# Kernel tuning notes

Hardware: AMD Instinct MI355X
Metric: run time of the kernel (lower is better)

The kernel has to match this reference:

```python
import jax, jax.numpy as jnp
import numpy as np
from math import comb

N_DEGREE = 3  # init kwarg n


def _exponent_nk(n, K):
    # Faithful port of exponent_nk: exponent rows of all degree-n monomials in K vars.
    ident = np.diag(np.ones(K))
    exp = ident
    for i in range(1, n):
        rows = []
        for j in range(K):
            for k in range(exp.shape[0] - comb(i + K - j - 1, i), exp.shape[0]):
                rows.append(ident[j, :] + exp[k, :])
        exp = np.stack(rows, axis=0)
    return exp


def _mono_indices(powers):
    # For each exponent row, list the variable indices with multiplicity (deg entries).
    M, K = powers.shape
    deg = int(powers[0].sum())
    idx = np.zeros((M, deg), dtype=np.int32)
    for i in range(M):
        c = 0
        for j in range(K):
            for _ in range(int(powers[i, j])):
                idx[i, c] = j
                c += 1
    return idx


def _generate_veronese(x, n):
    # x: (K, N). Returns (D, N) with rows [1; x; deg2 monomials; ...; degn monomials].
    K, N = x.shape
    parts = [jnp.ones((1, N), x.dtype), x]
    for deg in range(2, n + 1):
        idx = _mono_indices(_exponent_nk(deg, K))  # (M, deg) static int indices
        y = x[idx[:, 0]]  # (M, N)
        for t in range(1, deg):
            y = y * x[idx[:, t]]
        parts.append(y)
    return jnp.concatenate(parts, axis=0)


def reference(x, M_inv):
    npoints, dims = x.shape
    # Faithful to torch: .view is a row-major reshape, NOT a transpose.
    xr = jnp.reshape(x, (dims, npoints))
    v = _generate_veronese(xr, N_DEGREE)  # (D, N)
    D, N = v.shape
    vq = jnp.reshape(v, (N, D))  # faithful replica of v_x.view(BS, 1, D)
    t = vq @ M_inv               # (N, D)
    out = jnp.sum(t * vq, axis=1)  # (N,) quadratic form v^T M_inv v
    return out.reshape(N, 1, 1)


def setup_inputs() -> dict:
    key = jax.random.key(0)
    k1, k2 = jax.random.split(key)
    npoints, dims = 262144, 10
    D = comb(dims + N_DEGREE, N_DEGREE)  # 286
    x = jax.random.normal(k1, (npoints, dims), dtype=jnp.float32)
    M_inv = jax.random.normal(k2, (D, D), dtype=jnp.float32)
    return {"x": x, "M_inv": M_inv}
```

## Files before the change

kernel.cpp:

```cpp
#include <hip/hip_runtime.h>
#include <hip/hip_bf16.h>
#include <stdint.h>

#define NLOG 18
#define NMASK ((1u << NLOG) - 1u)
#define RSTRB 592u
#define ROWS 32u
#define TPB 384u
#define MPB (ROWS * 286u)

typedef __attribute__((ext_vector_type(8))) short short8;
typedef __attribute__((ext_vector_type(4))) float f32x4;
typedef f32x4 uf32x4 __attribute__((aligned(4)));

struct Tab { uint16_t v[286]; };
constexpr Tab make_tab() {
  Tab t{};
  int idx = 0;
  t.v[idx++] = 0;
  for (int a = 0; a < 10; ++a) t.v[idx++] = (uint16_t)(a + 1);
  for (int a = 0; a < 10; ++a)
    for (int b = a; b < 10; ++b) t.v[idx++] = (uint16_t)((a + 1) | ((b + 1) << 4));
  for (int a = 0; a < 10; ++a)
    for (int b = a; b < 10; ++b)
      for (int c = b; c < 10; ++c)
        t.v[idx++] = (uint16_t)((a + 1) | ((b + 1) << 4) | ((c + 1) << 8));
  return t;
}
__constant__ Tab g_tab = make_tab();

__device__ uint4 g_bpack[11520];

__device__ __forceinline__ uint32_t f2bf(float f) {
  uint32_t u = __float_as_uint(f);
  return (u + 0x7FFFu + ((u >> 16) & 1u)) >> 16;
}
__device__ __forceinline__ float bf2f(uint32_t u) { return __uint_as_float(u << 16); }
__device__ __forceinline__ uint32_t pk2bf(float lo, float hi) {
  __hip_bfloat162 h2 = __float22bfloat162_rn(make_float2(lo, hi));
  return *(uint32_t*)&h2;
}

__global__ __launch_bounds__(256) void prep_kernel(const float* __restrict__ M) {
  uint32_t t = blockIdx.x * 256u + threadIdx.x;
  uint32_t k0 = t / 1280u;
  uint32_t r = t - k0 * 1280u;
  uint32_t g = r / 320u;
  uint32_t e = r - g * 320u;
  uint32_t kb = k0 * 32u + g * 8u;
  float v[8];
#pragma unroll
  for (int i = 0; i < 8; ++i) {
    uint32_t k = kb + (uint32_t)i;
    v[i] = (k < 286u && e < 286u) ? M[k * 286u + e] : 0.f;
  }
  uint4 o;
  o.x = f2bf(v[0]) | (f2bf(v[1]) << 16);
  o.y = f2bf(v[2]) | (f2bf(v[3]) << 16);
  o.z = f2bf(v[4]) | (f2bf(v[5]) << 16);
  o.w = f2bf(v[6]) | (f2bf(v[7]) << 16);
  g_bpack[t] = o;
}

__device__ __forceinline__ float mono1(const float* __restrict__ x, uint32_t tv, uint32_t j) {
  float val = 1.f;
  int a = (int)(tv & 15u) - 1;
  if (a >= 0) {
    val = x[((uint32_t)a << NLOG) + j];
    int b = (int)((tv >> 4) & 15u) - 1;
    if (b >= 0) {
      val *= x[((uint32_t)b << NLOG) + j];
      int c = (int)(tv >> 8) - 1;
      if (c >= 0) val *= x[((uint32_t)c << NLOG) + j];
    }
  }
  return val;
}

__global__ __launch_bounds__(TPB, 6) void qform_kernel(const float* __restrict__ x,
                                                       float* __restrict__ out) {
  extern __shared__ char smem[];
  float* part = (float*)(smem + 18944);

  const uint32_t tid = threadIdx.x;
  const uint32_t wid = tid >> 6, lane = tid & 63u;
  const uint32_t n0 = blockIdx.x * ROWS;
  const uint32_t mb = blockIdx.x * MPB;

  for (uint32_t it = 0; it < 6u; ++it) {
    uint32_t t4 = it * TPB + tid;
    if (t4 >= 2272u) break;
    uint32_t row = t4 / 71u;
    uint32_t grp = t4 - row * 71u;
    uint32_t d0 = grp * 4u;
    uint32_t m0 = mb + row * 286u + d0;
    uint32_t i = m0 >> NLOG;
    if (__builtin_expect((m0 + 3u) >> NLOG == i, 1)) {
      uint32_t j0 = m0 & NMASK;
      uint32_t tv = g_tab.v[i];
      float pr[4];
      int a = (int)(tv & 15u) - 1;
      if (a >= 0) {
        uf32x4 va = *(const uf32x4*)(x + ((uint32_t)a << NLOG) + j0);
        pr[0] = va.x; pr[1] = va.y; pr[2] = va.z; pr[3] = va.w;
        int b = (int)((tv >> 4) & 15u) - 1;
        if (b >= 0) {
          uf32x4 vb = *(const uf32x4*)(x + ((uint32_t)b << NLOG) + j0);
          pr[0] *= vb.x; pr[1] *= vb.y; pr[2] *= vb.z; pr[3] *= vb.w;
          int c = (int)(tv >> 8) - 1;
          if (c >= 0) {
            uf32x4 vc = *(const uf32x4*)(x + ((uint32_t)c << NLOG) + j0);
            pr[0] *= vc.x; pr[1] *= vc.y; pr[2] *= vc.z; pr[3] *= vc.w;
          }
        }
      } else {
        pr[0] = 1.f; pr[1] = 1.f; pr[2] = 1.f; pr[3] = 1.f;
      }
      uint2 w01;
      w01.x = pk2bf(pr[0], pr[1]);
      w01.y = pk2bf(pr[2], pr[3]);
      *(uint2*)(smem + row * RSTRB + d0 * 2u) = w01;
    } else {
#pragma unroll
      for (uint32_t u = 0; u < 4u; ++u) {
        uint32_t m = m0 + u;
        float val = mono1(x, g_tab.v[m >> NLOG], m & NMASK);
        *(uint16_t*)(smem + row * RSTRB + (d0 + u) * 2u) = (uint16_t)f2bf(val);
      }
    }
  }
  if (tid < ROWS) {
    uint32_t row = tid;
#pragma unroll
    for (uint32_t u = 0; u < 2u; ++u) {
      uint32_t m = mb + row * 286u + 284u + u;
      float val = mono1(x, g_tab.v[m >> NLOG], m & NMASK);
      *(uint16_t*)(smem + row * RSTRB + (284u + u) * 2u) = (uint16_t)f2bf(val);
    }
    *(uint32_t*)(smem + row * RSTRB + 572u) = 0u;
  }

  const uint32_t we = wid;
  const uint32_t ag = lane >> 4;
  const uint32_t al = lane & 15u;
  const uint4* bbase = g_bpack + ag * 320u + we * 48u + al;
  const char* arow0 = smem + al * RSTRB;
  const char* arow1 = smem + (16u + al) * RSTRB;

  short8 bA[3];
#pragma unroll
  for (uint32_t fe = 0; fe < 3u; ++fe) bA[fe] = *(const short8*)(bbase + fe * 16u);

  f32x4 acc[2][3];
#pragma unroll
  for (int rf = 0; rf < 2; ++rf)
#pragma unroll
    for (int fe = 0; fe < 3; ++fe) acc[rf][fe] = (f32x4){0.f, 0.f, 0.f, 0.f};

  __syncthreads();

#pragma unroll 1
  for (uint32_t kp = 0; kp < 4u; ++kp) {
    const uint32_t k0 = 2u * kp;
    short8 bB[3];
#pragma unroll
    for (uint32_t fe = 0; fe < 3u; ++fe)
      bB[fe] = *(const short8*)(bbase + (k0 + 1u) * 1280u + fe * 16u);
    {
      short8 a0 = *(const short8*)(arow0 + (k0 * 4u + ag) * 16u);
      short8 a1 = *(const short8*)(arow1 + (k0 * 4u + ag) * 16u);
#pragma unroll
      for (int fe = 0; fe < 3; ++fe) {
        acc[0][fe] = __builtin_amdgcn_mfma_f32_16x16x32_bf16(a0, bA[fe], acc[0][fe], 0, 0, 0);
        acc[1][fe] = __builtin_amdgcn_mfma_f32_16x16x32_bf16(a1, bA[fe], acc[1][fe], 0, 0, 0);
      }
    }
#pragma unroll
    for (uint32_t fe = 0; fe < 3u; ++fe)
      bA[fe] = *(const short8*)(bbase + (k0 + 2u) * 1280u + fe * 16u);
    {
      short8 a0 = *(const short8*)(arow0 + ((k0 + 1u) * 4u + ag) * 16u);
      short8 a1 = *(const short8*)(arow1 + ((k0 + 1u) * 4u + ag) * 16u);
#pragma unroll
      for (int fe = 0; fe < 3; ++fe) {
        acc[0][fe] = __builtin_amdgcn_mfma_f32_16x16x32_bf16(a0, bB[fe], acc[0][fe], 0, 0, 0);
        acc[1][fe] = __builtin_amdgcn_mfma_f32_16x16x32_bf16(a1, bB[fe], acc[1][fe], 0, 0, 0);
      }
    }
  }
  {
    short8 a0 = *(const short8*)(arow0 + (32u + ag) * 16u);
    short8 a1 = *(const short8*)(arow1 + (32u + ag) * 16u);
#pragma unroll
    for (int fe = 0; fe < 3; ++fe) {
      acc[0][fe] = __builtin_amdgcn_mfma_f32_16x16x32_bf16(a0, bA[fe], acc[0][fe], 0, 0, 0);
      acc[1][fe] = __builtin_amdgcn_mfma_f32_16x16x32_bf16(a1, bA[fe], acc[1][fe], 0, 0, 0);
    }
  }

  float rs[2][4];
#pragma unroll
  for (uint32_t rf = 0; rf < 2u; ++rf) {
#pragma unroll
    for (uint32_t i = 0; i < 4u; ++i) {
      uint32_t r = rf * 16u + ag * 4u + i;
      float s = 0.f;
#pragma unroll
      for (uint32_t fe = 0; fe < 3u; ++fe) {
        uint32_t e = we * 48u + fe * 16u + al;
        float wv = bf2f(*(const uint16_t*)(smem + r * RSTRB + e * 2u));
        s = fmaf(acc[rf][fe][i], wv, s);
      }
      rs[rf][i] = s;
    }
  }
#pragma unroll
  for (uint32_t rf = 0; rf < 2u; ++rf)
#pragma unroll
    for (uint32_t i = 0; i < 4u; ++i) {
      float s = rs[rf][i];
      s += __shfl_xor(s, 1); s += __shfl_xor(s, 2);
      s += __shfl_xor(s, 4); s += __shfl_xor(s, 8);
      rs[rf][i] = s;
    }
  if (al == 0u) {
#pragma unroll
    for (uint32_t rf = 0; rf < 2u; ++rf)
#pragma unroll
      for (uint32_t i = 0; i < 4u; ++i)
        part[we * 32u + rf * 16u + ag * 4u + i] = rs[rf][i];
  }
  __syncthreads();
  if (tid < ROWS) {
    float o = 0.f;
#pragma unroll
    for (uint32_t w = 0; w < 6u; ++w) o += part[w * 32u + tid];
    out[n0 + tid] = o;
  }
}

extern "C" void kernel_launch(void* const* d_in, const int* in_sizes, int n_in,
                              void* d_out, int out_size, void* d_ws, size_t ws_size,
                              hipStream_t stream) {
  const float* x = (const float*)d_in[0];
  const float* M = (const float*)d_in[1];
  float* out = (float*)d_out;
  (void)in_sizes; (void)n_in; (void)out_size; (void)d_ws; (void)ws_size;
  prep_kernel<<<45, 256, 0, stream>>>(M);
  qform_kernel<<<8192, TPB, 19712, stream>>>(x, out);
}
```

Baseline: 177.3 us.

## Widen monomial build to 8 per thread and drop B double-buffering

The Veronese build stage now makes each thread produce 8 monomials with paired 16-byte loads and a single 16-byte LDS store. It fully unrolls 3 iterations and folds the tail and zero-padding work into the main loop. The K-loop loses its ping-pong B register buffer, with B fragments loaded just before use, and launch bounds ask for 7 waves per SIMD to cut register pressure and raise occupancy. The trade is less latency hiding for global B loads inside the MFMA loop and a larger unaligned global-load footprint per thread.

After: 164.0 us. 1.08x faster.

```diff
diff --git a/kernel.cpp b/kernel.cpp
--- a/kernel.cpp
+++ b/kernel.cpp
@@ -11,7 +11,7 @@
 
 typedef __attribute__((ext_vector_type(8))) short short8;
 typedef __attribute__((ext_vector_type(4))) float f32x4;
-typedef f32x4 uf32x4 __attribute__((aligned(4)));
+typedef f32x4 uf32x4 __attribute__((aligned(8)));
 
 struct Tab { uint16_t v[286]; };
 constexpr Tab make_tab() {
@@ -77,7 +77,7 @@
   return val;
 }
 
-__global__ __launch_bounds__(TPB, 6) void qform_kernel(const float* __restrict__ x,
+__global__ __launch_bounds__(TPB, 7) void qform_kernel(const float* __restrict__ x,
                                                        float* __restrict__ out) {
   extern __shared__ char smem[];
   float* part = (float*)(smem + 18944);
@@ -87,57 +87,59 @@
   const uint32_t n0 = blockIdx.x * ROWS;
   const uint32_t mb = blockIdx.x * MPB;
 
-  for (uint32_t it = 0; it < 6u; ++it) {
+#pragma unroll
+  for (uint32_t it = 0; it < 3u; ++it) {
     uint32_t t4 = it * TPB + tid;
-    if (t4 >= 2272u) break;
-    uint32_t row = t4 / 71u;
-    uint32_t grp = t4 - row * 71u;
-    uint32_t d0 = grp * 4u;
+    uint32_t row = t4 / 36u;
+    uint32_t grp = t4 - row * 36u;
+    uint32_t d0 = grp * 8u;
     uint32_t m0 = mb + row * 286u + d0;
     uint32_t i = m0 >> NLOG;
-    if (__builtin_expect((m0 + 3u) >> NLOG == i, 1)) {
+    bool lastg = (grp == 35u);
+    if (__builtin_expect((m0 + 7u) >> NLOG == i, 1)) {
       uint32_t j0 = m0 & NMASK;
       uint32_t tv = g_tab.v[i];
-      float pr[4];
+      float pr[8];
       int a = (int)(tv & 15u) - 1;
       if (a >= 0) {
-        uf32x4 va = *(const uf32x4*)(x + ((uint32_t)a << NLOG) + j0);
-        pr[0] = va.x; pr[1] = va.y; pr[2] = va.z; pr[3] = va.w;
+        const uf32x4* xa = (const uf32x4*)(x + ((uint32_t)a << NLOG) + j0);
+        uf32x4 lo = xa[0], hi = xa[1];
+        pr[0] = lo.x; pr[1] = lo.y; pr[2] = lo.z; pr[3] = lo.w;
+        pr[4] = hi.x; pr[5] = hi.y; pr[6] = hi.z; pr[7] = hi.w;
         int b = (int)((tv >> 4) & 15u) - 1;
         if (b >= 0) {
-          uf32x4 vb = *(const uf32x4*)(x + ((uint32_t)b << NLOG) + j0);
-          pr[0] *= vb.x; pr[1] *= vb.y; pr[2] *= vb.z; pr[3] *= vb.w;
+          const uf32x4* xb = (const uf32x4*)(x + ((uint32_t)b << NLOG) + j0);
+          uf32x4 lo2 = xb[0], hi2 = xb[1];
+          pr[0] *= lo2.x; pr[1] *= lo2.y; pr[2] *= lo2.z; pr[3] *= lo2.w;
+          pr[4] *= hi2.x; pr[5] *= hi2.y; pr[6] *= hi2.z; pr[7] *= hi2.w;
           int c = (int)(tv >> 8) - 1;
           if (c >= 0) {
-            uf32x4 vc = *(const uf32x4*)(x + ((uint32_t)c << NLOG) + j0);
-            pr[0] *= vc.x; pr[1] *= vc.y; pr[2] *= vc.z; pr[3] *= vc.w;
+            const uf32x4* xc = (const uf32x4*)(x + ((uint32_t)c << NLOG) + j0);
+            uf32x4 lo3 = xc[0], hi3 = xc[1];
+            pr[0] *= lo3.x; pr[1] *= lo3.y; pr[2] *= lo3.z; pr[3] *= lo3.w;
+            pr[4] *= hi3.x; pr[5] *= hi3.y; pr[6] *= hi3.z; pr[7] *= hi3.w;
           }
         }
       } else {
-        pr[0] = 1.f; pr[1] = 1.f; pr[2] = 1.f; pr[3] = 1.f;
+#pragma unroll
+        for (int u = 0; u < 8; ++u) pr[u] = 1.f;
       }
-      uint2 w01;
-      w01.x = pk2bf(pr[0], pr[1]);
-      w01.y = pk2bf(pr[2], pr[3]);
-      *(uint2*)(smem + row * RSTRB + d0 * 2u) = w01;
+      uint4 w4;
+      w4.x = pk2bf(pr[0], pr[1]);
+      w4.y = pk2bf(pr[2], pr[3]);
+      w4.z = pk2bf(pr[4], pr[5]);
+      w4.w = lastg ? 0u : pk2bf(pr[6], pr[7]);
+      *(uint4*)(smem + row * RSTRB + d0 * 2u) = w4;
     } else {
 #pragma unroll
-      for (uint32_t u = 0; u < 4u; ++u) {
+      for (uint32_t u = 0; u < 8u; ++u) {
+        uint32_t d = d0 + u;
         uint32_t m = m0 + u;
-        float val = mono1(x, g_tab.v[m >> NLOG], m & NMASK);
-        *(uint16_t*)(smem + row * RSTRB + (d0 + u) * 2u) = (uint16_t)f2bf(val);
+        uint16_t hv = 0;
+        if (d < 286u) hv = (uint16_t)f2bf(mono1(x, g_tab.v[m >> NLOG], m & NMASK));
+        *(uint16_t*)(smem + row * RSTRB + d * 2u) = hv;
       }
     }
-  }
-  if (tid < ROWS) {
-    uint32_t row = tid;
-#pragma unroll
-    for (uint32_t u = 0; u < 2u; ++u) {
-      uint32_t m = mb + row * 286u + 284u + u;
-      float val = mono1(x, g_tab.v[m >> NLOG], m & NMASK);
-      *(uint16_t*)(smem + row * RSTRB + (284u + u) * 2u) = (uint16_t)f2bf(val);
-    }
-    *(uint32_t*)(smem + row * RSTRB + 572u) = 0u;
   }
 
   const uint32_t we = wid;
@@ -147,9 +149,9 @@
   const char* arow0 = smem + al * RSTRB;
   const char* arow1 = smem + (16u + al) * RSTRB;
 
-  short8 bA[3];
-#pragma unroll
-  for (uint32_t fe = 0; fe < 3u; ++fe) bA[fe] = *(const short8*)(bbase + fe * 16u);
+  short8 b[3];
+#pragma unroll
+  for (uint32_t fe = 0; fe < 3u; ++fe) b[fe] = *(const short8*)(bbase + fe * 16u);
 
   f32x4 acc[2][3];
 #pragma unroll
@@ -159,42 +161,26 @@
 
   __syncthreads();
 
+  {
+    short8 a0 = *(const short8*)(arow0 + ag * 16u);
+    short8 a1 = *(const short8*)(arow1 + ag * 16u);
+#pragma unroll
+    for (int fe = 0; fe < 3; ++fe) {
+      acc[0][fe] = __builtin_amdgcn_mfma_f32_16x16x32_bf16(a0, b[fe], acc[0][fe], 0, 0, 0);
+      acc[1][fe] = __builtin_amdgcn_mfma_f32_16x16x32_bf16(a1, b[fe], acc[1][fe], 0, 0, 0);
+    }
+  }
 #pragma unroll 1
-  for (uint32_t kp = 0; kp < 4u; ++kp) {
-    const uint32_t k0 = 2u * kp;
-    short8 bB[3];
+  for (uint32_t k0 = 1; k0 < 9u; ++k0) {
 #pragma unroll
     for (uint32_t fe = 0; fe < 3u; ++fe)
-      bB[fe] = *(const short8*)(bbase + (k0 + 1u) * 1280u + fe * 16u);
-    {
-      short8 a0 = *(const short8*)(arow0 + (k0 * 4u + ag) * 16u);
-      short8 a1 = *(const short8*)(arow1 + (k0 * 4u + ag) * 16u);
-#pragma unroll
-      for (int fe = 0; fe < 3; ++fe) {
-        acc[0][fe] = __builtin_amdgcn_mfma_f32_16x16x32_bf16(a0, bA[fe], acc[0][fe], 0, 0, 0);
-        acc[1][fe] = __builtin_amdgcn_mfma_f32_16x16x32_bf16(a1, bA[fe], acc[1][fe], 0, 0, 0);
-      }
-    }
-#pragma unroll
-    for (uint32_t fe = 0; fe < 3u; ++fe)
-      bA[fe] = *(const short8*)(bbase + (k0 + 2u) * 1280u + fe * 16u);
-    {
-      short8 a0 = *(const short8*)(arow0 + ((k0 + 1u) * 4u + ag) * 16u);
-      short8 a1 = *(const short8*)(arow1 + ((k0 + 1u) * 4u + ag) * 16u);
-#pragma unroll
-      for (int fe = 0; fe < 3; ++fe) {
-        acc[0][fe] = __builtin_amdgcn_mfma_f32_16x16x32_bf16(a0, bB[fe], acc[0][fe], 0, 0, 0);
-        acc[1][fe] = __builtin_amdgcn_mfma_f32_16x16x32_bf16(a1, bB[fe], acc[1][fe], 0, 0, 0);
-      }
-    }
-  }
-  {
-    short8 a0 = *(const short8*)(arow0 + (32u + ag) * 16u);
-    short8 a1 = *(const short8*)(arow1 + (32u + ag) * 16u);
+      b[fe] = *(const short8*)(bbase + k0 * 1280u + fe * 16u);
+    short8 a0 = *(const short8*)(arow0 + (k0 * 4u + ag) * 16u);
+    short8 a1 = *(const short8*)(arow1 + (k0 * 4u + ag) * 16u);
 #pragma unroll
     for (int fe = 0; fe < 3; ++fe) {
-      acc[0][fe] = __builtin_amdgcn_mfma_f32_16x16x32_bf16(a0, bA[fe], acc[0][fe], 0, 0, 0);
-      acc[1][fe] = __builtin_amdgcn_mfma_f32_16x16x32_bf16(a1, bA[fe], acc[1][fe], 0, 0, 0);
+      acc[0][fe] = __builtin_amdgcn_mfma_f32_16x16x32_bf16(a0, b[fe], acc[0][fe], 0, 0, 0);
+      acc[1][fe] = __builtin_amdgcn_mfma_f32_16x16x32_bf16(a1, b[fe], acc[1][fe], 0, 0, 0);
     }
   }
 
```
